# Kernel tuning notes

Measured on AMD Instinct MI355X. Metric: run time of the kernel, lower is better.

## Reference

```python
import jax, jax.numpy as jnp
import numpy as np

SEQ_LEN = 4096
EMBED = 1024
HIDDEN = 128
BATCH = 8


def setup_inputs() -> dict:
    key = jax.random.key(0)
    k_in, k_q, k_k, k_v = jax.random.split(key, 4)
    inputs = jax.random.normal(k_in, (BATCH, SEQ_LEN, EMBED), dtype=jnp.float32)
    # nn.Linear(embed, hidden, bias=False) weights; stored [hidden, embed] in torch,
    # we keep [embed, hidden] for x @ W.
    scale = 1.0 / np.sqrt(EMBED)
    Wq = jax.random.uniform(k_q, (EMBED, HIDDEN), jnp.float32, -scale, scale)
    Wk = jax.random.uniform(k_k, (EMBED, HIDDEN), jnp.float32, -scale, scale)
    Wv = jax.random.uniform(k_v, (EMBED, HIDDEN), jnp.float32, -scale, scale)
    return {"inputs": inputs, "Wq": Wq, "Wk": Wk, "Wv": Wv}


def reference(inputs, Wq, Wk, Wv):
    # Single-head causal scaled dot-product attention.
    q = jnp.einsum("bse,eh->bsh", inputs, Wq)
    k = jnp.einsum("bse,eh->bsh", inputs, Wk)
    v = jnp.einsum("bse,eh->bsh", inputs, Wv)
    d_k = q.shape[-1]
    q = q / jnp.sqrt(jnp.asarray(d_k, q.dtype))
    scores = jnp.einsum("bqh,bkh->bqk", q, k)  # [B, S, S]
    seq = scores.shape[-1]
    causal = jnp.tril(jnp.ones((seq, seq), dtype=bool))
    scores = jnp.where(causal, scores, jnp.asarray(-jnp.inf, scores.dtype))
    weights = jax.nn.softmax(scores, axis=-1)
    return jnp.einsum("bqk,bkh->bqh", weights, v)
```

## Files before the change

kernel.cpp:

```cpp
#include <hip/hip_runtime.h>
#include <stdint.h>

#define B_ 8
#define S_ 4096
#define E_ 1024
#define H_ 128
#define M_ (B_*S_)

typedef __attribute__((ext_vector_type(8))) short short8;
typedef __attribute__((ext_vector_type(4))) float f32x4;
typedef __attribute__((ext_vector_type(16))) float f32x16;

static constexpr float QSCALE = 0.08838834764831845f;

__device__ __forceinline__ unsigned short f2bf(float f) {
    uint32_t u = __float_as_uint(f);
    u += 0x7fffu + ((u >> 16) & 1u);
    return (unsigned short)(u >> 16);
}

__device__ __forceinline__ uint32_t cvt_pk_bf16(float a, float b) {
    uint32_t r;
    asm("v_cvt_pk_bf16_f32 %0, %1, %2" : "=v"(r) : "v"(a), "v"(b));
    return r;
}

__device__ __forceinline__ void gl16(const void* g, void* s) {
    __builtin_amdgcn_global_load_lds(
        (const __attribute__((address_space(1))) unsigned int*)g,
        (__attribute__((address_space(3))) unsigned int*)s, 16, 0, 0);
}

__global__ __launch_bounds__(256)
void prep_w_kernel(const float* __restrict__ Wq, const float* __restrict__ Wk,
                   const float* __restrict__ Wv, unsigned short* __restrict__ Wt)
{
    int id = blockIdx.x*256 + threadIdx.x;
    int which = id >> 14;
    int rem = id & 16383;
    int h = rem >> 7, kc = rem & 127;
    const float* __restrict__ W = (which==0)?Wq:((which==1)?Wk:Wv);
    const float scale = (which==0)? QSCALE : 1.0f;
    uint32_t u[4];
    #pragma unroll
    for (int p=0;p<4;++p) {
        unsigned short a = f2bf(W[(size_t)(kc*8 + 2*p  )*H_ + h] * scale);
        unsigned short b = f2bf(W[(size_t)(kc*8 + 2*p+1)*H_ + h] * scale);
        u[p] = (uint32_t)a | ((uint32_t)b << 16);
    }
    uint4 v; v.x=u[0]; v.y=u[1]; v.z=u[2]; v.w=u[3];
    int gp = (kc >> 2)*64 + ((((kc & 3) + ((h >> 1) & 3)) & 3) * 16);
    *(uint4*)((unsigned char*)Wt + (size_t)(which*H_ + h)*2048 + gp) = v;
}

__device__ __forceinline__ void proj_stage(unsigned char* buf,
                                           const unsigned char* xb,
                                           const unsigned char* Wb,
                                           int i, int w, int l)
{
    #pragma unroll
    for (int j=0;j<4;++j) {
        int cb = w*4096 + j*1024;
        int A  = cb + (l << 4);
        if (cb < 8192) {
            int row = A >> 7, col = A & 127;
            gl16(xb + (size_t)row*4096 + i*128 + (col ^ ((row & 7) << 4)), buf + cb);
        } else {
            int A2 = A - 8192;
            int wr = A2 >> 6, w6 = A2 & 63;
            gl16(Wb + (size_t)wr*2048 + i*64 + w6, buf + cb);
        }
    }
}

__global__ __launch_bounds__(512)
void proj_kernel(const float* __restrict__ x, const unsigned short* __restrict__ Wt,
                 unsigned short* __restrict__ Qg, unsigned short* __restrict__ Kg,
                 unsigned short* __restrict__ Vtg)
{
    const int t = threadIdx.x;
    const int w = t >> 6, l = t & 63;
    const int grp = l >> 4, li = l & 15;
    const int rg = w & 1, cg = w >> 1;
    const int rb = blockIdx.x;
    const int row0 = rb * 64;

    __shared__ __align__(128) unsigned char smem[65536];
    unsigned short* epi = (unsigned short*)smem;

    const unsigned char* xb = (const unsigned char*)x + (size_t)row0*4096;
    const unsigned char* Wb = (const unsigned char*)Wt;

    f32x4 acc[2][6];
    const f32x4 zz = {0.f,0.f,0.f,0.f};
    #pragma unroll
    for (int mt=0;mt<2;++mt)
        #pragma unroll
        for (int nt=0;nt<6;++nt) acc[mt][nt] = zz;

    proj_stage(smem, xb, Wb, 0, w, l);
    __syncthreads();

    int cur = 0;
    for (int i=0; i<32; ++i) {
        if (i+1 < 32) proj_stage(smem + (cur^1)*32768, xb, Wb, i+1, w, l);

        const unsigned char* sX = smem + cur*32768;
        const unsigned char* sW = sX + 8192;

        short8 af[2];
        #pragma unroll
        for (int mt=0;mt<2;++mt) {
            int row = rg*32 + mt*16 + li;
            int sw = (row & 7) << 4;
            float4 a0 = *(const float4*)(sX + row*128 + ((grp*32     ) ^ sw));
            float4 a1 = *(const float4*)(sX + row*128 + ((grp*32 + 16) ^ sw));
            union { uint32_t u[4]; short8 s; } pa;
            pa.u[0] = cvt_pk_bf16(a0.x, a0.y);
            pa.u[1] = cvt_pk_bf16(a0.z, a0.w);
            pa.u[2] = cvt_pk_bf16(a1.x, a1.y);
            pa.u[3] = cvt_pk_bf16(a1.z, a1.w);
            af[mt] = pa.s;
        }
        #pragma unroll
        for (int nt=0;nt<6;++nt) {
            int wr = cg*96 + nt*16 + li;
            short8 bf = *(const short8*)(sW + wr*64 + (((grp + (wr >> 1)) & 3) << 4));
            acc[0][nt] = __builtin_amdgcn_mfma_f32_16x16x32_bf16(af[0], bf, acc[0][nt], 0,0,0);
            acc[1][nt] = __builtin_amdgcn_mfma_f32_16x16x32_bf16(af[1], bf, acc[1][nt], 0,0,0);
        }

        __syncthreads();
        cur ^= 1;
    }

    const int bidx = rb >> 6;
    const int srow = (rb & 63) * 64;

    if (cg < 2) {
        #pragma unroll
        for (int mt=0;mt<2;++mt)
            #pragma unroll
            for (int nt=0;nt<6;++nt)
                #pragma unroll
                for (int r=0;r<4;++r) {
                    int rowl = rg*32 + mt*16 + grp*4 + r;
                    int col  = cg*96 + nt*16 + li;
                    epi[rowl*208 + col] = f2bf(acc[mt][nt][r]);
                }
    }
    __syncthreads();
    #pragma unroll
    for (int i=0;i<2;++i) {
        int idx = i*512 + t;
        int row = idx >> 4, cc = idx & 15;
        uint4 v = *(const uint4*)((const unsigned char*)epi + row*416 + cc*16);
        *(uint4*)((unsigned char*)Qg + (size_t)(row0+row)*256 + cc*16) = v;
    }
    {
        int row = t >> 3, cc = t & 7;
        uint4 v = *(const uint4*)((const unsigned char*)epi + row*416 + 256 + cc*16);
        *(uint4*)((unsigned char*)Kg + (size_t)(row0+row)*256 + cc*16) = v;
    }
    __syncthreads();

    if (cg >= 2) {
        #pragma unroll
        for (int mt=0;mt<2;++mt)
            #pragma unroll
            for (int nt=0;nt<6;++nt)
                #pragma unroll
                for (int r=0;r<4;++r) {
                    int rowl = rg*32 + mt*16 + grp*4 + r;
                    int col  = (cg-2)*96 + nt*16 + li;
                    epi[rowl*208 + col] = f2bf(acc[mt][nt][r]);
                }
    }
    __syncthreads();
    {
        int row = t >> 3, cc = t & 7;
        uint4 v = *(const uint4*)((const unsigned char*)epi + row*416 + cc*16);
        *(uint4*)((unsigned char*)Kg + (size_t)(row0+row)*256 + 128 + cc*16) = v;
    }
    #pragma unroll
    for (int i=0;i<2;++i) {
        int idx = i*512 + t;
        int h = idx >> 3, sc = idx & 7;
        uint32_t u[4];
        #pragma unroll
        for (int p=0;p<4;++p) {
            unsigned short a = epi[(sc*8 + 2*p    )*208 + 64 + h];
            unsigned short b = epi[(sc*8 + 2*p + 1)*208 + 64 + h];
            u[p] = (uint32_t)a | ((uint32_t)b << 16);
        }
        uint4 v; v.x=u[0]; v.y=u[1]; v.z=u[2]; v.w=u[3];
        *(uint4*)(Vtg + (size_t)(bidx*H_ + h)*S_ + srow + sc*8) = v;
    }
}

__device__ __forceinline__ void stage_tile(unsigned char* buf,
                                           const unsigned char* Kb,
                                           const unsigned char* Vb,
                                           int kt, int w, int l)
{
    unsigned char* sVb = buf + 16384;
    #pragma unroll
    for (int j=0;j<2;++j) {
        int A = w*2048 + j*1024 + (l<<4);
        int krow = A >> 8;
        int kin  = A & 255;
        gl16(Kb + (size_t)kt*16384 + krow*256 + (kin ^ ((krow&7)<<4)),
             buf + w*2048 + j*1024);
        int h   = A >> 7;
        int vin = A & 127;
        gl16(Vb + (size_t)h*8192 + (size_t)kt*128 + (vin ^ ((h&7)<<4)),
             sVb + w*2048 + j*1024);
    }
}

__global__ __launch_bounds__(512, 2)
void attn_p1(const unsigned short* __restrict__ Qg,
             const unsigned short* __restrict__ Kg,
             const unsigned short* __restrict__ Vtg,
             float* __restrict__ Pp, float* __restrict__ Ml)
{
    const int t    = threadIdx.x;
    const int w    = t >> 6;
    const int l    = t & 63;
    const int hi   = l >> 5;
    const int c31  = l & 31;
    const int gid  = blockIdx.x;
    const int b    = gid & 7;
    const int rr   = gid >> 3;
    const int c4   = rr & 3;
    const int pr   = rr >> 2;

    __shared__ __align__(128) unsigned char smem[65536];

    const size_t bbase = (size_t)b * S_ * H_;
    const unsigned char* Kb = (const unsigned char*)(Kg + bbase);
    const unsigned char* Vb = (const unsigned char*)(Vtg + (size_t)b*H_*S_);
    const int swzq = (c31 & 7) << 4;

    int cur = 0;
    for (int ph = 0; ph < 2; ++ph) {
        const int qt   = ph ? (15 - pr) : pr;
        const int q0   = qt * 256;
        const int qw0  = q0 + w*32;
        const int qrow = qw0 + c31;
        const int nkt  = 4*(qt+1);

        short8 qf[8];
        {
            const unsigned short* qp = Qg + bbase + (size_t)qrow * H_;
            #pragma unroll
            for (int ks=0; ks<8; ++ks)
                qf[ks] = *(const short8*)(qp + ks*16 + hi*8);
        }

        f32x16 oacc[4];
        #pragma unroll
        for (int ht=0; ht<4; ++ht)
            #pragma unroll
            for (int r=0; r<16; ++r) oacc[ht][r] = 0.f;
        float mrun = -1e30f, lrun = 0.f;

        stage_tile(smem + cur*32768, Kb, Vb, c4, w, l);
        __syncthreads();

        for (int kt = c4; kt < nkt; kt += 4) {
            const bool pre = (kt+4 < nkt);
            if (pre) stage_tile(smem + (cur^1)*32768, Kb, Vb, kt+4, w, l);

            if (kt*64 <= qw0 + 31) {
                const unsigned char* sK = smem + cur*32768;
                const unsigned char* sV = sK + 16384;

                f32x16 sacc[2];
                #pragma unroll
                for (int st=0; st<2; ++st)
                    #pragma unroll
                    for (int r=0; r<16; ++r) sacc[st][r] = 0.f;
                #pragma unroll
                for (int st=0; st<2; ++st) {
                    int krow = st*32 + c31;
                    #pragma unroll
                    for (int ks=0; ks<8; ++ks) {
                        short8 kf = *(const short8*)(sK + krow*256 + ((ks*32 + hi*16) ^ swzq));
                        sacc[st] = __builtin_amdgcn_mfma_f32_32x32x16_bf16(kf, qf[ks], sacc[st], 0,0,0);
                    }
                }

                if (kt*64 + 63 > qw0) {
                    #pragma unroll
                    for (int st=0; st<2; ++st)
                        #pragma unroll
                        for (int r=0; r<16; ++r) {
                            int key = kt*64 + st*32 + (r&3) + 8*(r>>2) + 4*hi;
                            if (key > qrow) sacc[st][r] = -1e30f;
                        }
                }

                float pmax = -1e30f;
                #pragma unroll
                for (int st=0; st<2; ++st)
                    #pragma unroll
                    for (int r=0; r<16; ++r) pmax = fmaxf(pmax, sacc[st][r]);
                pmax = fmaxf(pmax, __shfl_xor(pmax, 32, 64));

                if (!__all(pmax - mrun <= 8.0f)) {
                    float mnew = fmaxf(mrun, pmax);
                    float alpha = __expf(mrun - mnew);
                    #pragma unroll
                    for (int ht=0; ht<4; ++ht)
                        #pragma unroll
                        for (int r=0; r<16; ++r) oacc[ht][r] *= alpha;
                    lrun *= alpha;
                    mrun = mnew;
                }

                float p[2][16];
                float psum = 0.f;
                #pragma unroll
                for (int st=0; st<2; ++st)
                    #pragma unroll
                    for (int r=0; r<16; ++r) {
                        float e = __expf(sacc[st][r] - mrun);
                        p[st][r] = e;
                        psum += e;
                    }
                psum += __shfl_xor(psum, 32, 64);
                lrun += psum;

                short8 pf[4];
                #pragma unroll
                for (int st=0; st<2; ++st) {
                    uint32_t A0 = cvt_pk_bf16(p[st][0],  p[st][1]);
                    uint32_t A1 = cvt_pk_bf16(p[st][2],  p[st][3]);
                    uint32_t B0 = cvt_pk_bf16(p[st][4],  p[st][5]);
                    uint32_t B1 = cvt_pk_bf16(p[st][6],  p[st][7]);
                    uint32_t C0 = cvt_pk_bf16(p[st][8],  p[st][9]);
                    uint32_t C1 = cvt_pk_bf16(p[st][10], p[st][11]);
                    uint32_t D0 = cvt_pk_bf16(p[st][12], p[st][13]);
                    uint32_t D1 = cvt_pk_bf16(p[st][14], p[st][15]);
                    {
                        uint32_t x0 = hi ? A0 : B0;
                        uint32_t x1 = hi ? A1 : B1;
                        uint32_t y0 = (uint32_t)__shfl_xor((int)x0, 32, 64);
                        uint32_t y1 = (uint32_t)__shfl_xor((int)x1, 32, 64);
                        union { uint32_t u[4]; short8 s; } uu;
                        uu.u[0] = hi ? y0 : A0;
                        uu.u[1] = hi ? y1 : A1;
                        uu.u[2] = hi ? B0 : y0;
                        uu.u[3] = hi ? B1 : y1;
                        pf[st*2] = uu.s;
                    }
                    {
                        uint32_t x0 = hi ? C0 : D0;
                        uint32_t x1 = hi ? C1 : D1;
                        uint32_t y0 = (uint32_t)__shfl_xor((int)x0, 32, 64);
                        uint32_t y1 = (uint32_t)__shfl_xor((int)x1, 32, 64);
                        union { uint32_t u[4]; short8 s; } uu;
                        uu.u[0] = hi ? y0 : C0;
                        uu.u[1] = hi ? y1 : C1;
                        uu.u[2] = hi ? D0 : y0;
                        uu.u[3] = hi ? D1 : y1;
                        pf[st*2+1] = uu.s;
                    }
                }

                #pragma unroll
                for (int sl=0; sl<4; ++sl) {
                    #pragma unroll
                    for (int ht=0; ht<4; ++ht) {
                        int h = ht*32 + c31;
                        short8 vf = *(const short8*)(sV + h*128 + ((sl*32 + hi*16) ^ swzq));
                        oacc[ht] = __builtin_amdgcn_mfma_f32_32x32x16_bf16(vf, pf[sl], oacc[ht], 0,0,0);
                    }
                }
            }

            __syncthreads();
            if (pre) cur ^= 1;
        }

        float* Prow = Pp + (size_t)c4*((size_t)M_*H_) + bbase + (size_t)qrow*H_;
        #pragma unroll
        for (int ht=0; ht<4; ++ht)
            #pragma unroll
            for (int k=0; k<4; ++k) {
                float4 o;
                o.x = oacc[ht][4*k+0];
                o.y = oacc[ht][4*k+1];
                o.z = oacc[ht][4*k+2];
                o.w = oacc[ht][4*k+3];
                *(float4*)(Prow + ht*32 + 8*k + 4*hi) = o;
            }
        if (hi == 0) {
            float2 ml2; ml2.x = mrun; ml2.y = lrun;
            *(float2*)(Ml + ((size_t)c4*M_ + (size_t)b*S_ + qrow)*2) = ml2;
        }
    }
}

__global__ __launch_bounds__(256)
void attn_merge(const float* __restrict__ Pp, const float* __restrict__ Ml,
                float* __restrict__ Out)
{
    int gid = blockIdx.x*256 + threadIdx.x;
    int q  = gid >> 5;
    int h4 = gid & 31;

    float m0 = Ml[((size_t)0*M_ + q)*2], l0 = Ml[((size_t)0*M_ + q)*2 + 1];
    float m1 = Ml[((size_t)1*M_ + q)*2], l1 = Ml[((size_t)1*M_ + q)*2 + 1];
    float m2 = Ml[((size_t)2*M_ + q)*2], l2 = Ml[((size_t)2*M_ + q)*2 + 1];
    float m3 = Ml[((size_t)3*M_ + q)*2], l3 = Ml[((size_t)3*M_ + q)*2 + 1];

    float M = fmaxf(fmaxf(m0, m1), fmaxf(m2, m3));
    float w0 = __expf(m0 - M), w1 = __expf(m1 - M);
    float w2 = __expf(m2 - M), w3 = __expf(m3 - M);
    float L = w0*l0 + w1*l1 + w2*l2 + w3*l3;

    float4 p0 = *(const float4*)(Pp + (size_t)0*((size_t)M_*H_) + (size_t)q*H_ + h4*4);
    float4 p1 = *(const float4*)(Pp + (size_t)1*((size_t)M_*H_) + (size_t)q*H_ + h4*4);
    float4 p2 = *(const float4*)(Pp + (size_t)2*((size_t)M_*H_) + (size_t)q*H_ + h4*4);
    float4 p3 = *(const float4*)(Pp + (size_t)3*((size_t)M_*H_) + (size_t)q*H_ + h4*4);
    float inv = 1.0f / L;
    float4 o;
    o.x = (w0*p0.x + w1*p1.x + w2*p2.x + w3*p3.x) * inv;
    o.y = (w0*p0.y + w1*p1.y + w2*p2.y + w3*p3.y) * inv;
    o.z = (w0*p0.z + w1*p1.z + w2*p2.z + w3*p3.z) * inv;
    o.w = (w0*p0.w + w1*p1.w + w2*p2.w + w3*p3.w) * inv;
    *(float4*)(Out + (size_t)q*H_ + h4*4) = o;
}

__global__ __launch_bounds__(128, 1)
void attn_fb(const unsigned short* __restrict__ Qg,
             const unsigned short* __restrict__ Kg,
             const unsigned short* __restrict__ Vtg,
             float* __restrict__ Out)
{
    const int t   = threadIdx.x;
    const int w   = t >> 6;
    const int l   = t & 63;
    const int hi  = l >> 5;
    const int c31 = l & 31;
    const int qt  = (S_/64 - 1) - blockIdx.x;
    const int b   = blockIdx.y;
    const int q0  = qt * 64;
    const int qrow = q0 + w*32 + c31;

    __shared__ __align__(128) unsigned char sK[16384];
    __shared__ __align__(128) unsigned char sV[16384];

    const size_t bbase = (size_t)b * S_ * H_;

    short8 qf[8];
    {
        const unsigned short* qp = Qg + bbase + (size_t)qrow * H_;
        #pragma unroll
        for (int ks=0; ks<8; ++ks)
            qf[ks] = *(const short8*)(qp + ks*16 + hi*8);
    }

    f32x16 oacc[4];
    #pragma unroll
    for (int ht=0; ht<4; ++ht)
        #pragma unroll
        for (int r=0; r<16; ++r) oacc[ht][r] = 0.f;
    float mrun = -1e30f, lrun = 0.f;

    const unsigned char* Kb = (const unsigned char*)(Kg + bbase);
    const unsigned char* Vb = (const unsigned char*)(Vtg + (size_t)b*H_*S_);
    const int swzq = (c31 & 7) << 4;

    for (int kt=0; kt<=qt; ++kt) {
        __syncthreads();
        #pragma unroll
        for (int i=0;i<8;++i) {
            int c = i*128 + t;
            int row = c >> 4, cb = (c & 15) * 16;
            *(uint4*)(sK + row*256 + (cb ^ ((row&7)<<4))) =
                *(const uint4*)(Kb + (size_t)(kt*64 + row)*256 + cb);
        }
        #pragma unroll
        for (int i=0;i<8;++i) {
            int c = i*128 + t;
            int h = c >> 3, cb = (c & 7) * 16;
            *(uint4*)(sV + h*128 + (cb ^ ((h&7)<<4))) =
                *(const uint4*)(Vb + (size_t)h*(S_*2) + kt*128 + cb);
        }
        __syncthreads();

        f32x16 sacc[2];
        #pragma unroll
        for (int st=0; st<2; ++st)
            #pragma unroll
            for (int r=0; r<16; ++r) sacc[st][r] = 0.f;
        #pragma unroll
        for (int st=0; st<2; ++st) {
            int krow = st*32 + c31;
            #pragma unroll
            for (int ks=0; ks<8; ++ks) {
                short8 kf = *(const short8*)(sK + krow*256 + ((ks*32 + hi*16) ^ swzq));
                sacc[st] = __builtin_amdgcn_mfma_f32_32x32x16_bf16(kf, qf[ks], sacc[st], 0,0,0);
            }
        }

        if (kt == qt) {
            #pragma unroll
            for (int st=0; st<2; ++st)
                #pragma unroll
                for (int r=0; r<16; ++r) {
                    int key = q0 + st*32 + (r&3) + 8*(r>>2) + 4*hi;
                    if (key > qrow) sacc[st][r] = -1e30f;
                }
        }

        float pmax = -1e30f;
        #pragma unroll
        for (int st=0; st<2; ++st)
            #pragma unroll
            for (int r=0; r<16; ++r) pmax = fmaxf(pmax, sacc[st][r]);
        pmax = fmaxf(pmax, __shfl_xor(pmax, 32, 64));

        if (!__all(pmax - mrun <= 8.0f)) {
            float mnew = fmaxf(mrun, pmax);
            float alpha = __expf(mrun - mnew);
            #pragma unroll
            for (int ht=0; ht<4; ++ht)
                #pragma unroll
                for (int r=0; r<16; ++r) oacc[ht][r] *= alpha;
            lrun *= alpha;
            mrun = mnew;
        }

        float p[2][16];
        float psum = 0.f;
        #pragma unroll
        for (int st=0; st<2; ++st)
            #pragma unroll
            for (int r=0; r<16; ++r) {
                float e = __expf(sacc[st][r] - mrun);
                p[st][r] = e;
                psum += e;
            }
        psum += __shfl_xor(psum, 32, 64);
        lrun += psum;

        short8 pf[4];
        #pragma unroll
        for (int st=0; st<2; ++st) {
            uint32_t A0 = cvt_pk_bf16(p[st][0],  p[st][1]);
            uint32_t A1 = cvt_pk_bf16(p[st][2],  p[st][3]);
            uint32_t B0 = cvt_pk_bf16(p[st][4],  p[st][5]);
            uint32_t B1 = cvt_pk_bf16(p[st][6],  p[st][7]);
            uint32_t C0 = cvt_pk_bf16(p[st][8],  p[st][9]);
            uint32_t C1 = cvt_pk_bf16(p[st][10], p[st][11]);
            uint32_t D0 = cvt_pk_bf16(p[st][12], p[st][13]);
            uint32_t D1 = cvt_pk_bf16(p[st][14], p[st][15]);
            {
                uint32_t x0 = hi ? A0 : B0;
                uint32_t x1 = hi ? A1 : B1;
                uint32_t y0 = (uint32_t)__shfl_xor((int)x0, 32, 64);
                uint32_t y1 = (uint32_t)__shfl_xor((int)x1, 32, 64);
                union { uint32_t u[4]; short8 s; } uu;
                uu.u[0] = hi ? y0 : A0;
                uu.u[1] = hi ? y1 : A1;
                uu.u[2] = hi ? B0 : y0;
                uu.u[3] = hi ? B1 : y1;
                pf[st*2] = uu.s;
            }
            {
                uint32_t x0 = hi ? C0 : D0;
                uint32_t x1 = hi ? C1 : D1;
                uint32_t y0 = (uint32_t)__shfl_xor((int)x0, 32, 64);
                uint32_t y1 = (uint32_t)__shfl_xor((int)x1, 32, 64);
                union { uint32_t u[4]; short8 s; } uu;
                uu.u[0] = hi ? y0 : C0;
                uu.u[1] = hi ? y1 : C1;
                uu.u[2] = hi ? D0 : y0;
                uu.u[3] = hi ? D1 : y1;
                pf[st*2+1] = uu.s;
            }
        }

        #pragma unroll
        for (int sl=0; sl<4; ++sl) {
            #pragma unroll
            for (int ht=0; ht<4; ++ht) {
                int h = ht*32 + c31;
                short8 vf = *(const short8*)(sV + h*128 + ((sl*32 + hi*16) ^ swzq));
                oacc[ht] = __builtin_amdgcn_mfma_f32_32x32x16_bf16(vf, pf[sl], oacc[ht], 0,0,0);
            }
        }
    }

    float linv = 1.0f / lrun;
    float* Op = Out + bbase + (size_t)qrow * H_;
    #pragma unroll
    for (int ht=0; ht<4; ++ht)
        #pragma unroll
        for (int k=0; k<4; ++k) {
            float4 o;
            o.x = oacc[ht][4*k+0] * linv;
            o.y = oacc[ht][4*k+1] * linv;
            o.z = oacc[ht][4*k+2] * linv;
            o.w = oacc[ht][4*k+3] * linv;
            *(float4*)(Op + ht*32 + 8*k + 4*hi) = o;
        }
}

extern "C" void kernel_launch(void* const* d_in, const int* in_sizes, int n_in,
                              void* d_out, int out_size, void* d_ws, size_t ws_size,
                              hipStream_t stream) {
    const float* x  = (const float*)d_in[0];
    const float* Wq = (const float*)d_in[1];
    const float* Wk = (const float*)d_in[2];
    const float* Wv = (const float*)d_in[3];

    unsigned char* ws = (unsigned char*)d_ws;
    unsigned short* Wt  = (unsigned short*)ws;
    unsigned short* Qg  = (unsigned short*)(ws + 1048576u);
    unsigned short* Kg  = (unsigned short*)(ws + 9437184u);
    unsigned short* Vtg = (unsigned short*)(ws + 17825792u);
    float* Pp = (float*)(ws + 26214400u);
    float* Ml = (float*)(ws + 93323264u);
    const size_t NEED = 94371840u;

    prep_w_kernel<<<192, 256, 0, stream>>>(Wq, Wk, Wv, Wt);
    proj_kernel<<<512, 512, 0, stream>>>(x, Wt, Qg, Kg, Vtg);

    if (ws_size >= NEED) {
        attn_p1<<<256, 512, 0, stream>>>(Qg, Kg, Vtg, Pp, Ml);
        attn_merge<<<4096, 256, 0, stream>>>(Pp, Ml, (float*)d_out);
    } else {
        dim3 ga(S_/64, B_);
        attn_fb<<<ga, 128, 0, stream>>>(Qg, Kg, Vtg, (float*)d_out);
    }
}
```

Baseline: 115.5 us.

## Split projection kernel across output-column halves to double block count

The QKV projection kernel now launches twice as many blocks, each computing half of the 384 output columns (Q plus half of K, or the other half of K plus V) for a 64-row tile. Shared memory per block shrinks from 64KB to 40KB and the accumulator count halves. This targets the low occupancy of 512 blocks on a 256-CU device and the serialized two-pass epilogue. In exchange, each x tile is read from global memory twice, once per column half.

```diff
diff --git a/kernel.cpp b/kernel.cpp
--- a/kernel.cpp
+++ b/kernel.cpp
@@ -55,12 +55,13 @@
 
 __device__ __forceinline__ void proj_stage(unsigned char* buf,
                                            const unsigned char* xb,
-                                           const unsigned char* Wb,
+                                           const unsigned char* Wb2,
                                            int i, int w, int l)
 {
     #pragma unroll
-    for (int j=0;j<4;++j) {
-        int cb = w*4096 + j*1024;
+    for (int j=0;j<3;++j) {
+        int cb = (j*8 + w) * 1024;
+        if (cb >= 20480) continue;
         int A  = cb + (l << 4);
         if (cb < 8192) {
             int row = A >> 7, col = A & 127;
@@ -68,7 +69,7 @@
         } else {
             int A2 = A - 8192;
             int wr = A2 >> 6, w6 = A2 & 63;
-            gl16(Wb + (size_t)wr*2048 + i*64 + w6, buf + cb);
+            gl16(Wb2 + (size_t)wr*2048 + i*64 + w6, buf + cb);
         }
     }
 }
@@ -82,30 +83,31 @@
     const int w = t >> 6, l = t & 63;
     const int grp = l >> 4, li = l & 15;
     const int rg = w & 1, cg = w >> 1;
-    const int rb = blockIdx.x;
+    const int bid = blockIdx.x;
+    const int rb = bid >> 1, half = bid & 1;
     const int row0 = rb * 64;
 
-    __shared__ __align__(128) unsigned char smem[65536];
+    __shared__ __align__(128) unsigned char smem[40960];
     unsigned short* epi = (unsigned short*)smem;
 
-    const unsigned char* xb = (const unsigned char*)x + (size_t)row0*4096;
-    const unsigned char* Wb = (const unsigned char*)Wt;
-
-    f32x4 acc[2][6];
+    const unsigned char* xb  = (const unsigned char*)x + (size_t)row0*4096;
+    const unsigned char* Wb2 = (const unsigned char*)Wt + (size_t)half*192*2048;
+
+    f32x4 acc[2][3];
     const f32x4 zz = {0.f,0.f,0.f,0.f};
     #pragma unroll
     for (int mt=0;mt<2;++mt)
         #pragma unroll
-        for (int nt=0;nt<6;++nt) acc[mt][nt] = zz;
-
-    proj_stage(smem, xb, Wb, 0, w, l);
+        for (int nt=0;nt<3;++nt) acc[mt][nt] = zz;
+
+    proj_stage(smem, xb, Wb2, 0, w, l);
     __syncthreads();
 
     int cur = 0;
     for (int i=0; i<32; ++i) {
-        if (i+1 < 32) proj_stage(smem + (cur^1)*32768, xb, Wb, i+1, w, l);
-
-        const unsigned char* sX = smem + cur*32768;
+        if (i+1 < 32) proj_stage(smem + (cur^1)*20480, xb, Wb2, i+1, w, l);
+
+        const unsigned char* sX = smem + cur*20480;
         const unsigned char* sW = sX + 8192;
 
         short8 af[2];
@@ -123,8 +125,8 @@
             af[mt] = pa.s;
         }
         #pragma unroll
-        for (int nt=0;nt<6;++nt) {
-            int wr = cg*96 + nt*16 + li;
+        for (int nt=0;nt<3;++nt) {
+            int wr = cg*48 + nt*16 + li;
             short8 bf = *(const short8*)(sW + wr*64 + (((grp + (wr >> 1)) & 3) << 4));
             acc[0][nt] = __builtin_amdgcn_mfma_f32_16x16x32_bf16(af[0], bf, acc[0][nt], 0,0,0);
             acc[1][nt] = __builtin_amdgcn_mfma_f32_16x16x32_bf16(af[1], bf, acc[1][nt], 0,0,0);
@@ -137,64 +139,51 @@
     const int bidx = rb >> 6;
     const int srow = (rb & 63) * 64;
 
-    if (cg < 2) {
-        #pragma unroll
-        for (int mt=0;mt<2;++mt)
-            #pragma unroll
-            for (int nt=0;nt<6;++nt)
-                #pragma unroll
-                for (int r=0;r<4;++r) {
-                    int rowl = rg*32 + mt*16 + grp*4 + r;
-                    int col  = cg*96 + nt*16 + li;
-                    epi[rowl*208 + col] = f2bf(acc[mt][nt][r]);
-                }
-    }
+    #pragma unroll
+    for (int mt=0;mt<2;++mt)
+        #pragma unroll
+        for (int nt=0;nt<3;++nt)
+            #pragma unroll
+            for (int r=0;r<4;++r) {
+                int rowl = rg*32 + mt*16 + grp*4 + r;
+                int col  = cg*48 + nt*16 + li;
+                epi[rowl*200 + col] = f2bf(acc[mt][nt][r]);
+            }
     __syncthreads();
-    #pragma unroll
-    for (int i=0;i<2;++i) {
-        int idx = i*512 + t;
-        int row = idx >> 4, cc = idx & 15;
-        uint4 v = *(const uint4*)((const unsigned char*)epi + row*416 + cc*16);
-        *(uint4*)((unsigned char*)Qg + (size_t)(row0+row)*256 + cc*16) = v;
-    }
-    {
-        int row = t >> 3, cc = t & 7;
-        uint4 v = *(const uint4*)((const unsigned char*)epi + row*416 + 256 + cc*16);
-        *(uint4*)((unsigned char*)Kg + (size_t)(row0+row)*256 + cc*16) = v;
-    }
-    __syncthreads();
-
-    if (cg >= 2) {
-        #pragma unroll
-        for (int mt=0;mt<2;++mt)
-            #pragma unroll
-            for (int nt=0;nt<6;++nt)
-                #pragma unroll
-                for (int r=0;r<4;++r) {
-                    int rowl = rg*32 + mt*16 + grp*4 + r;
-                    int col  = (cg-2)*96 + nt*16 + li;
-                    epi[rowl*208 + col] = f2bf(acc[mt][nt][r]);
-                }
-    }
-    __syncthreads();
-    {
-        int row = t >> 3, cc = t & 7;
-        uint4 v = *(const uint4*)((const unsigned char*)epi + row*416 + cc*16);
-        *(uint4*)((unsigned char*)Kg + (size_t)(row0+row)*256 + 128 + cc*16) = v;
-    }
-    #pragma unroll
-    for (int i=0;i<2;++i) {
-        int idx = i*512 + t;
-        int h = idx >> 3, sc = idx & 7;
-        uint32_t u[4];
-        #pragma unroll
-        for (int p=0;p<4;++p) {
-            unsigned short a = epi[(sc*8 + 2*p    )*208 + 64 + h];
-            unsigned short b = epi[(sc*8 + 2*p + 1)*208 + 64 + h];
-            u[p] = (uint32_t)a | ((uint32_t)b << 16);
-        }
-        uint4 v; v.x=u[0]; v.y=u[1]; v.z=u[2]; v.w=u[3];
-        *(uint4*)(Vtg + (size_t)(bidx*H_ + h)*S_ + srow + sc*8) = v;
+
+    if (half == 0) {
+        #pragma unroll
+        for (int i=0;i<2;++i) {
+            int idx = i*512 + t;
+            int row = idx >> 4, cc = idx & 15;
+            uint4 v = *(const uint4*)((const unsigned char*)epi + row*400 + cc*16);
+            *(uint4*)((unsigned char*)Qg + (size_t)(row0+row)*256 + cc*16) = v;
+        }
+        {
+            int row = t >> 3, cc = t & 7;
+            uint4 v = *(const uint4*)((const unsigned char*)epi + row*400 + 256 + cc*16);
+            *(uint4*)((unsigned char*)Kg + (size_t)(row0+row)*256 + cc*16) = v;
+        }
+    } else {
+        {
+            int row = t >> 3, cc = t & 7;
+            uint4 v = *(const uint4*)((const unsigned char*)epi + row*400 + cc*16);
+            *(uint4*)((unsigned char*)Kg + (size_t)(row0+row)*256 + 128 + cc*16) = v;
+        }
+        #pragma unroll
+        for (int i=0;i<2;++i) {
+            int idx = i*512 + t;
+            int h = idx >> 3, sc = idx & 7;
+            uint32_t u[4];
+            #pragma unroll
+            for (int p=0;p<4;++p) {
+                unsigned short a = epi[(sc*8 + 2*p    )*200 + 64 + h];
+                unsigned short b = epi[(sc*8 + 2*p + 1)*200 + 64 + h];
+                u[p] = (uint32_t)a | ((uint32_t)b << 16);
+            }
+            uint4 v; v.x=u[0]; v.y=u[1]; v.z=u[2]; v.w=u[3];
+            *(uint4*)(Vtg + (size_t)(bidx*H_ + h)*S_ + srow + sc*8) = v;
+        }
     }
 }
 
@@ -629,7 +618,7 @@
     const size_t NEED = 94371840u;
 
     prep_w_kernel<<<192, 256, 0, stream>>>(Wq, Wk, Wv, Wt);
-    proj_kernel<<<512, 512, 0, stream>>>(x, Wt, Qg, Kg, Vtg);
+    proj_kernel<<<1024, 512, 0, stream>>>(x, Wt, Qg, Kg, Vtg);
 
     if (ws_size >= NEED) {
         attn_p1<<<256, 512, 0, stream>>>(Qg, Kg, Vtg, Pp, Ml);
```

After: 128.8 us. 1.12x slower.

## Store split-K attention partials in bf16 and use single-buffered wider K tiles in projection

Applied to the files above, without the earlier changes.

The attention partial outputs written by attn_p1 and read back by attn_merge are stored as bf16 instead of fp32, which halves that intermediate's traffic and shrinks the workspace. The projection kernel switches from a double-buffered 32-step loop over 128-byte K slices to a single-buffered 16-step loop over 256-byte slices. The weight layout's swizzle changes to match. This trades load/compute overlap for fewer iterations and barriers, and the bf16 partials lose some precision before the merge.

```diff
diff --git a/kernel.cpp b/kernel.cpp
--- a/kernel.cpp
+++ b/kernel.cpp
@@ -23,6 +23,10 @@
     uint32_t r;
     asm("v_cvt_pk_bf16_f32 %0, %1, %2" : "=v"(r) : "v"(a), "v"(b));
     return r;
+}
+
+__device__ __forceinline__ float bf2f(uint32_t u) {
+    return __uint_as_float(u << 16);
 }
 
 __device__ __forceinline__ void gl16(const void* g, void* s) {
@@ -49,7 +53,7 @@
         u[p] = (uint32_t)a | ((uint32_t)b << 16);
     }
     uint4 v; v.x=u[0]; v.y=u[1]; v.z=u[2]; v.w=u[3];
-    int gp = (kc >> 2)*64 + ((((kc & 3) + ((h >> 1) & 3)) & 3) * 16);
+    int gp = (kc >> 3)*128 + (((kc & 7) ^ (h & 7)) << 4);
     *(uint4*)((unsigned char*)Wt + (size_t)(which*H_ + h)*2048 + gp) = v;
 }
 
@@ -59,16 +63,19 @@
                                            int i, int w, int l)
 {
     #pragma unroll
-    for (int j=0;j<4;++j) {
-        int cb = w*4096 + j*1024;
+    for (int j=0;j<8;++j) {
+        int cb = (j*8 + w) * 1024;
         int A  = cb + (l << 4);
-        if (cb < 8192) {
-            int row = A >> 7, col = A & 127;
-            gl16(xb + (size_t)row*4096 + i*128 + (col ^ ((row & 7) << 4)), buf + cb);
+        if (cb < 16384) {
+            int sub = A >> 13;
+            int A2  = A & 8191;
+            int row = A2 >> 7, col = A2 & 127;
+            gl16(xb + (size_t)row*4096 + i*256 + sub*128 + (col ^ ((row & 7) << 4)),
+                 buf + cb);
         } else {
-            int A2 = A - 8192;
-            int wr = A2 >> 6, w6 = A2 & 63;
-            gl16(Wb + (size_t)wr*2048 + i*64 + w6, buf + cb);
+            int A2 = A - 16384;
+            int wr = A2 >> 7, wc = A2 & 127;
+            gl16(Wb + (size_t)wr*2048 + i*128 + wc, buf + cb);
         }
     }
 }
@@ -101,37 +108,40 @@
     proj_stage(smem, xb, Wb, 0, w, l);
     __syncthreads();
 
-    int cur = 0;
-    for (int i=0; i<32; ++i) {
-        if (i+1 < 32) proj_stage(smem + (cur^1)*32768, xb, Wb, i+1, w, l);
-
-        const unsigned char* sX = smem + cur*32768;
-        const unsigned char* sW = sX + 8192;
-
-        short8 af[2];
-        #pragma unroll
-        for (int mt=0;mt<2;++mt) {
-            int row = rg*32 + mt*16 + li;
-            int sw = (row & 7) << 4;
-            float4 a0 = *(const float4*)(sX + row*128 + ((grp*32     ) ^ sw));
-            float4 a1 = *(const float4*)(sX + row*128 + ((grp*32 + 16) ^ sw));
-            union { uint32_t u[4]; short8 s; } pa;
-            pa.u[0] = cvt_pk_bf16(a0.x, a0.y);
-            pa.u[1] = cvt_pk_bf16(a0.z, a0.w);
-            pa.u[2] = cvt_pk_bf16(a1.x, a1.y);
-            pa.u[3] = cvt_pk_bf16(a1.z, a1.w);
-            af[mt] = pa.s;
-        }
-        #pragma unroll
-        for (int nt=0;nt<6;++nt) {
-            int wr = cg*96 + nt*16 + li;
-            short8 bf = *(const short8*)(sW + wr*64 + (((grp + (wr >> 1)) & 3) << 4));
-            acc[0][nt] = __builtin_amdgcn_mfma_f32_16x16x32_bf16(af[0], bf, acc[0][nt], 0,0,0);
-            acc[1][nt] = __builtin_amdgcn_mfma_f32_16x16x32_bf16(af[1], bf, acc[1][nt], 0,0,0);
+    for (int i=0; i<16; ++i) {
+        const unsigned char* sX = smem;
+        const unsigned char* sW = smem + 16384;
+
+        #pragma unroll
+        for (int ks=0;ks<2;++ks) {
+            short8 af[2];
+            #pragma unroll
+            for (int mt=0;mt<2;++mt) {
+                int row = rg*32 + mt*16 + li;
+                int sw = (row & 7) << 4;
+                float4 a0 = *(const float4*)(sX + ks*8192 + row*128 + ((grp*32     ) ^ sw));
+                float4 a1 = *(const float4*)(sX + ks*8192 + row*128 + ((grp*32 + 16) ^ sw));
+                union { uint32_t u[4]; short8 s; } pa;
+                pa.u[0] = cvt_pk_bf16(a0.x, a0.y);
+                pa.u[1] = cvt_pk_bf16(a0.z, a0.w);
+                pa.u[2] = cvt_pk_bf16(a1.x, a1.y);
+                pa.u[3] = cvt_pk_bf16(a1.z, a1.w);
+                af[mt] = pa.s;
+            }
+            #pragma unroll
+            for (int nt=0;nt<6;++nt) {
+                int wr = cg*96 + nt*16 + li;
+                short8 bf = *(const short8*)(sW + wr*128 + ((ks*64 + grp*16) ^ ((wr & 7) << 4)));
+                acc[0][nt] = __builtin_amdgcn_mfma_f32_16x16x32_bf16(af[0], bf, acc[0][nt], 0,0,0);
+                acc[1][nt] = __builtin_amdgcn_mfma_f32_16x16x32_bf16(af[1], bf, acc[1][nt], 0,0,0);
+            }
         }
 
         __syncthreads();
-        cur ^= 1;
+        if (i+1 < 16) {
+            proj_stage(smem, xb, Wb, i+1, w, l);
+            __syncthreads();
+        }
     }
 
     const int bidx = rb >> 6;
@@ -222,7 +232,7 @@
 void attn_p1(const unsigned short* __restrict__ Qg,
              const unsigned short* __restrict__ Kg,
              const unsigned short* __restrict__ Vtg,
-             float* __restrict__ Pp, float* __restrict__ Ml)
+             unsigned short* __restrict__ Pp, float* __restrict__ Ml)
 {
     const int t    = threadIdx.x;
     const int w    = t >> 6;
@@ -384,17 +394,15 @@
             if (pre) cur ^= 1;
         }
 
-        float* Prow = Pp + (size_t)c4*((size_t)M_*H_) + bbase + (size_t)qrow*H_;
+        unsigned short* Prow = Pp + (size_t)c4*((size_t)M_*H_) + bbase + (size_t)qrow*H_;
         #pragma unroll
         for (int ht=0; ht<4; ++ht)
             #pragma unroll
             for (int k=0; k<4; ++k) {
-                float4 o;
-                o.x = oacc[ht][4*k+0];
-                o.y = oacc[ht][4*k+1];
-                o.z = oacc[ht][4*k+2];
-                o.w = oacc[ht][4*k+3];
-                *(float4*)(Prow + ht*32 + 8*k + 4*hi) = o;
+                uint2 o;
+                o.x = cvt_pk_bf16(oacc[ht][4*k+0], oacc[ht][4*k+1]);
+                o.y = cvt_pk_bf16(oacc[ht][4*k+2], oacc[ht][4*k+3]);
+                *(uint2*)(Prow + ht*32 + 8*k + 4*hi) = o;
             }
         if (hi == 0) {
             float2 ml2; ml2.x = mrun; ml2.y = lrun;
@@ -404,7 +412,7 @@
 }
 
 __global__ __launch_bounds__(256)
-void attn_merge(const float* __restrict__ Pp, const float* __restrict__ Ml,
+void attn_merge(const unsigned short* __restrict__ Pp, const float* __restrict__ Ml,
                 float* __restrict__ Out)
 {
     int gid = blockIdx.x*256 + threadIdx.x;
@@ -421,16 +429,20 @@
     float w2 = __expf(m2 - M), w3 = __expf(m3 - M);
     float L = w0*l0 + w1*l1 + w2*l2 + w3*l3;
 
-    float4 p0 = *(const float4*)(Pp + (size_t)0*((size_t)M_*H_) + (size_t)q*H_ + h4*4);
-    float4 p1 = *(const float4*)(Pp + (size_t)1*((size_t)M_*H_) + (size_t)q*H_ + h4*4);
-    float4 p2 = *(const float4*)(Pp + (size_t)2*((size_t)M_*H_) + (size_t)q*H_ + h4*4);
-    float4 p3 = *(const float4*)(Pp + (size_t)3*((size_t)M_*H_) + (size_t)q*H_ + h4*4);
+    uint2 u0 = *(const uint2*)(Pp + (size_t)0*((size_t)M_*H_) + (size_t)q*H_ + h4*4);
+    uint2 u1 = *(const uint2*)(Pp + (size_t)1*((size_t)M_*H_) + (size_t)q*H_ + h4*4);
+    uint2 u2 = *(const uint2*)(Pp + (size_t)2*((size_t)M_*H_) + (size_t)q*H_ + h4*4);
+    uint2 u3 = *(const uint2*)(Pp + (size_t)3*((size_t)M_*H_) + (size_t)q*H_ + h4*4);
     float inv = 1.0f / L;
     float4 o;
-    o.x = (w0*p0.x + w1*p1.x + w2*p2.x + w3*p3.x) * inv;
-    o.y = (w0*p0.y + w1*p1.y + w2*p2.y + w3*p3.y) * inv;
-    o.z = (w0*p0.z + w1*p1.z + w2*p2.z + w3*p3.z) * inv;
-    o.w = (w0*p0.w + w1*p1.w + w2*p2.w + w3*p3.w) * inv;
+    o.x = (w0*bf2f(u0.x & 0xffffu) + w1*bf2f(u1.x & 0xffffu)
+         + w2*bf2f(u2.x & 0xffffu) + w3*bf2f(u3.x & 0xffffu)) * inv;
+    o.y = (w0*bf2f(u0.x >> 16)     + w1*bf2f(u1.x >> 16)
+         + w2*bf2f(u2.x >> 16)     + w3*bf2f(u3.x >> 16)) * inv;
+    o.z = (w0*bf2f(u0.y & 0xffffu) + w1*bf2f(u1.y & 0xffffu)
+         + w2*bf2f(u2.y & 0xffffu) + w3*bf2f(u3.y & 0xffffu)) * inv;
+    o.w = (w0*bf2f(u0.y >> 16)     + w1*bf2f(u1.y >> 16)
+         + w2*bf2f(u2.y >> 16)     + w3*bf2f(u3.y >> 16)) * inv;
     *(float4*)(Out + (size_t)q*H_ + h4*4) = o;
 }
 
@@ -624,9 +636,9 @@
     unsigned short* Qg  = (unsigned short*)(ws + 1048576u);
     unsigned short* Kg  = (unsigned short*)(ws + 9437184u);
     unsigned short* Vtg = (unsigned short*)(ws + 17825792u);
-    float* Pp = (float*)(ws + 26214400u);
-    float* Ml = (float*)(ws + 93323264u);
-    const size_t NEED = 94371840u;
+    unsigned short* Pp  = (unsigned short*)(ws + 26214400u);
+    float* Ml = (float*)(ws + 59768832u);
+    const size_t NEED = 60817408u;
 
     prep_w_kernel<<<192, 256, 0, stream>>>(Wq, Wk, Wv, Wt);
     proj_kernel<<<512, 512, 0, stream>>>(x, Wt, Qg, Kg, Vtg);
```

After: 105.4 us (median of 3 runs). -8.8%, faster.
